# Performance work log

Measured on AMD Instinct MI355X. Metric: run time of the kernel, lower is better.

The kernel has to match this reference:

```python
import jax, jax.numpy as jnp
import numpy as np
from jax.scipy.special import logsumexp


def _lstm(x, mask, Wk, Wr, b, reverse=False):
    # x: [B,T,D], mask: [B,T] bool. Keras LSTM defaults: gate order i,f,g,o,
    # sigmoid recurrent activation, tanh activation. Masked steps carry state.
    if reverse:
        x = x[:, ::-1]
        mask = mask[:, ::-1]
    B, T, _ = x.shape
    H = Wr.shape[0]
    xz = jnp.einsum('btd,dh->bth', x, Wk) + b  # [B,T,4H] input projections, done once

    def step(carry, inp):
        h, c = carry
        z_t, m = inp  # [B,4H], [B]
        z = z_t + h @ Wr
        i, f, g, o = jnp.split(z, 4, axis=-1)
        i = jax.nn.sigmoid(i)
        f = jax.nn.sigmoid(f)
        g = jnp.tanh(g)
        o = jax.nn.sigmoid(o)
        c_new = f * c + i * g
        h_new = o * jnp.tanh(c_new)
        m = m[:, None]
        h = jnp.where(m, h_new, h)
        c = jnp.where(m, c_new, c)
        return (h, c), h

    h0 = jnp.zeros((B, H), x.dtype)
    (_, _), hs = jax.lax.scan(step, (h0, h0), (xz.transpose(1, 0, 2), mask.T))
    hs = hs.transpose(1, 0, 2)  # [B,T,H]
    if reverse:
        hs = hs[:, ::-1]
    return hs


def _crf_log_likelihood(logits, tags, lengths, trans):
    # TFA crf_log_likelihood: sequence_score - log_norm (forward algorithm)
    B, T, C = logits.shape
    t_idx = jnp.arange(T)
    mask = t_idx[None, :] < lengths[:, None]  # [B,T]
    # unary score: sum_t logits[b,t,tags[b,t]] over valid t
    unary = jnp.take_along_axis(logits, tags[..., None], axis=2)[..., 0]
    unary = jnp.sum(jnp.where(mask, unary, 0.0), axis=1)
    # binary score: sum_t trans[tags[t], tags[t+1]] for t < len-1
    binary = trans[tags[:, :-1], tags[:, 1:]]  # [B,T-1]
    mask2 = t_idx[None, : T - 1] < (lengths - 1)[:, None]
    binary = jnp.sum(jnp.where(mask2, binary, 0.0), axis=1)
    # log normalizer via forward algorithm scan
    alpha0 = logits[:, 0]  # [B,C]

    def step(alpha, inp):
        logit_t, m = inp  # [B,C], [B]
        new = logsumexp(alpha[:, :, None] + trans[None], axis=1) + logit_t
        alpha = jnp.where(m[:, None], new, alpha)
        return alpha, None

    alpha, _ = jax.lax.scan(step, alpha0,
                            (logits[:, 1:].transpose(1, 0, 2), mask[:, 1:].T))
    log_norm = logsumexp(alpha, axis=1)
    return unary + binary - log_norm


def setup_inputs() -> dict:
    key = jax.random.key(0)
    ks = jax.random.split(key, 12)
    V, D, H, C, B, T = 30000, 300, 256, 9, 64, 512
    lengths = jax.random.randint(ks[0], (B,), T // 4, T + 1).astype(jnp.int32)
    valid = jnp.arange(T)[None, :] < lengths[:, None]
    inputs = (jax.random.randint(ks[1], (B, T), 1, V) * valid).astype(jnp.int32)
    targets = (jax.random.randint(ks[2], (B, T), 0, C) * valid).astype(jnp.int32)
    s = 0.05
    return {
        'inputs': inputs,
        'inputs_length': lengths,
        'targets': targets,
        'embedding': jax.random.normal(ks[3], (V, D), jnp.float32) * s,
        'Wk_f': jax.random.normal(ks[4], (D, 4 * H), jnp.float32) * s,
        'Wr_f': jax.random.normal(ks[5], (H, 4 * H), jnp.float32) * s,
        'b_f': jnp.zeros((4 * H,), jnp.float32),
        'Wk_b': jax.random.normal(ks[6], (D, 4 * H), jnp.float32) * s,
        'Wr_b': jax.random.normal(ks[7], (H, 4 * H), jnp.float32) * s,
        'b_b': jnp.zeros((4 * H,), jnp.float32),
        'dense_W': jax.random.normal(ks[8], (2 * H, C), jnp.float32) * s,
        'dense_b': jnp.zeros((C,), jnp.float32),
        'trans': jax.random.uniform(ks[9], (C, C), jnp.float32),
    }


def reference(inputs, inputs_length, targets, embedding, Wk_f, Wr_f, b_f,
              Wk_b, Wr_b, b_b, dense_W, dense_b, trans):
    T = inputs.shape[1]
    mask = jnp.arange(T)[None, :] < inputs_length[:, None]  # [B,T]
    emb = embedding[inputs]  # [B,T,D] (dropout is identity in inference)
    h_f = _lstm(emb, mask, Wk_f, Wr_f, b_f, reverse=False)
    h_b = _lstm(emb, mask, Wk_b, Wr_b, b_b, reverse=True)
    h = jnp.concatenate([h_f, h_b], axis=-1)  # [B,T,2H]
    logits = h @ dense_W + dense_b  # [B,T,C]
    log_likelihood = _crf_log_likelihood(logits, targets, inputs_length, trans)
    return logits, log_likelihood, trans
```

## Files before the change

### kernel.cpp

```cpp
#include <hip/hip_runtime.h>
#include <cstdint>
#include <cstddef>

typedef unsigned int  u32;
typedef unsigned short u16;
typedef _Float16 f16;
typedef _Float16 f16x2 __attribute__((ext_vector_type(2)));
typedef _Float16 half8 __attribute__((ext_vector_type(8)));
typedef float    f32x4v __attribute__((ext_vector_type(4)));
typedef int      i32x4 __attribute__((ext_vector_type(4)));

#define BATCH 64
#define TSEQ  512
#define DEMB  300
#define KPAD  320
#define HDIM  256
#define G4    1024
#define NCLS  9

__device__ __forceinline__ u32 packf16(float a, float b) {
  f16x2 v; v.x = (f16)a; v.y = (f16)b;
  return __builtin_bit_cast(u32, v);
}
__device__ __forceinline__ float f16f(u16 x) {
  return (float)__builtin_bit_cast(f16, x);
}
__device__ __forceinline__ float sigm_fast(float x) {
  return __builtin_amdgcn_rcpf(1.f + __expf(-x));
}
__device__ __forceinline__ float tanh_fast(float x) {
  float ax = __builtin_fabsf(x);
  float e = __expf(-2.f * ax);
  float t = (1.f - e) * __builtin_amdgcn_rcpf(1.f + e);
  return copysignf(t, x);
}

__global__ __launch_bounds__(256) void prep_k(
    const float* __restrict__ emb, u16* __restrict__ embf16,
    const float* __restrict__ Wk_f, const float* __restrict__ Wk_b,
    u16* __restrict__ wkt,
    const float* __restrict__ Wr_f, const float* __restrict__ Wr_b,
    signed char* __restrict__ wr8)
{
  const int bid = blockIdx.x;
  if (bid < 1875) {
    const int v  = bid * 16 + (threadIdx.x >> 4);
    const int kc = threadIdx.x & 15;
    uint2* __restrict__ dst = (uint2*)(embf16 + (size_t)v * KPAD + kc * 20);
    if (kc < 15) {
      const float4* __restrict__ src =
          (const float4*)(emb + (size_t)v * DEMB + kc * 20);
      float4 t0 = src[0], t1 = src[1], t2 = src[2], t3 = src[3], t4 = src[4];
      dst[0] = make_uint2(packf16(t0.x, t0.y), packf16(t0.z, t0.w));
      dst[1] = make_uint2(packf16(t1.x, t1.y), packf16(t1.z, t1.w));
      dst[2] = make_uint2(packf16(t2.x, t2.y), packf16(t2.z, t2.w));
      dst[3] = make_uint2(packf16(t3.x, t3.y), packf16(t3.z, t3.w));
      dst[4] = make_uint2(packf16(t4.x, t4.y), packf16(t4.z, t4.w));
    } else {
#pragma unroll
      for (int j = 0; j < 5; ++j) dst[j] = make_uint2(0u, 0u);
    }
    return;
  }
  const int t   = bid - 1875;
  const int dir = t >> 6;
  const int blk = t & 63;
  {
    const float* __restrict__ Wk = dir ? Wk_b : Wk_f;
    const int col = blk * 16 + (threadIdx.x >> 4);
    const int kc  = threadIdx.x & 15;
    u32* __restrict__ dst = (u32*)(wkt + ((size_t)dir * G4 + col) * KPAD + kc * 20);
    if (kc < 15) {
      float tmp[20];
#pragma unroll
      for (int j = 0; j < 20; ++j) tmp[j] = Wk[(size_t)(kc * 20 + j) * G4 + col];
#pragma unroll
      for (int j = 0; j < 10; ++j) dst[j] = packf16(tmp[2 * j], tmp[2 * j + 1]);
    } else {
#pragma unroll
      for (int j = 0; j < 10; ++j) dst[j] = 0u;
    }
  }
  {
    const float* __restrict__ Wr = dir ? Wr_b : Wr_f;
    const int col = blk * 16 + (threadIdx.x >> 4);
    const int k0  = (threadIdx.x & 15) * 16;
    float tmp[16];
#pragma unroll
    for (int j = 0; j < 16; ++j) tmp[j] = Wr[(size_t)(k0 + j) * G4 + col];
    u32 pw[4];
#pragma unroll
    for (int jj = 0; jj < 4; ++jj) {
      u32 p = 0;
#pragma unroll
      for (int b = 0; b < 4; ++b) {
        int q = (int)__builtin_rintf(tmp[4 * jj + b] * 512.f);
        q = q > 127 ? 127 : (q < -127 ? -127 : q);
        p |= ((u32)(q & 255)) << (8 * b);
      }
      pw[jj] = p;
    }
    *(uint4*)(wr8 + ((size_t)dir * G4 + col) * HDIM + k0) =
        make_uint4(pw[0], pw[1], pw[2], pw[3]);
  }
}

__global__ __launch_bounds__(256, 2) void xz_gemm_k(
    const int* __restrict__ inputs, const u16* __restrict__ wkt,
    const u16* __restrict__ embf16, const float* __restrict__ b_f,
    const float* __restrict__ b_b, u16* __restrict__ xz)
{
  __shared__ __align__(16) u16 Bs[64 * 328];
  const int tid  = threadIdx.x;
  const int wv   = tid >> 6, lane = tid & 63;
  const int quad = lane >> 4, fl = lane & 15;
  const int rb   = blockIdx.x * 64;

  {
    const int srow = tid >> 2, seg = (tid & 3) * 80;
    const int vrow = inputs[rb + srow];
    const u16* __restrict__ bsrc = embf16 + (size_t)vrow * KPAD + seg;
#pragma unroll
    for (int jj = 0; jj < 10; ++jj) {
      uint4 v = *(const uint4*)(bsrc + jj * 8);
      *(uint4*)&Bs[srow * 328 + seg + jj * 8] = v;
    }
  }
  __syncthreads();

#pragma unroll
  for (int grp = 0; grp < 4; ++grp) {
    f32x4v acc[4][2][4];
#pragma unroll
    for (int d = 0; d < 4; ++d)
#pragma unroll
      for (int i = 0; i < 2; ++i)
#pragma unroll
        for (int bt = 0; bt < 4; ++bt) acc[d][i][bt] = (f32x4v){0.f, 0.f, 0.f, 0.f};

#pragma unroll
    for (int kt = 0; kt < 10; ++kt) {
      half8 bf[4];
#pragma unroll
      for (int bt = 0; bt < 4; ++bt)
        bf[bt] = *(const half8*)&Bs[(bt * 16 + fl) * 328 + kt * 32 + quad * 8];
#pragma unroll
      for (int d = 0; d < 4; ++d) {
        const int dcb = grp * 4 + d;
        const int dir = dcb >> 3;
        const int cb1 = (dcb & 7) * 128;
        const u16* __restrict__ arow =
            wkt + ((size_t)(dir * G4) + cb1 + wv * 32 + fl) * KPAD + quad * 8;
#pragma unroll
        for (int i = 0; i < 2; ++i) {
          half8 af = *(const half8*)(arow + (size_t)(i * 16) * KPAD + kt * 32);
#pragma unroll
          for (int bt = 0; bt < 4; ++bt)
            acc[d][i][bt] = __builtin_amdgcn_mfma_f32_16x16x32_f16(
                af, bf[bt], acc[d][i][bt], 0, 0, 0);
        }
      }
    }

#pragma unroll
    for (int d = 0; d < 4; ++d) {
      const int dcb = grp * 4 + d;
      const int dir = dcb >> 3;
      const int cb1 = (dcb & 7) * 128;
      const float* __restrict__ bias = dir ? b_b : b_f;
#pragma unroll
      for (int bt = 0; bt < 4; ++bt) {
        const int row = rb + bt * 16 + fl;
        u16* __restrict__ orow = xz + ((size_t)(dir * BATCH * TSEQ) + row) * G4;
#pragma unroll
        for (int i = 0; i < 2; ++i) {
          const int mb = cb1 + wv * 32 + i * 16 + quad * 4;
          const float4 bb = *(const float4*)&bias[mb];
          f32x4v v = acc[d][i][bt];
          uint2 pk;
          pk.x = packf16(v[0] + bb.x, v[1] + bb.y);
          pk.y = packf16(v[2] + bb.z, v[3] + bb.w);
          *(uint2*)&orow[mb] = pk;
        }
      }
    }
  }
}

#define MFI(a, b, c) __builtin_amdgcn_mfma_i32_16x16x64_i8(a, b, c, 0, 0, 0)
#define LD8(g, ct, kc) (*(const i32x4*)(wr8w + (size_t)((g) * 256 + 32 * w + (ct) * 16 + l15) * HDIM + (kc) * 64 + q16))
#define DECL8(g, ct) \
  i32x4 W##g##ct##_0 = LD8(g, ct, 0), W##g##ct##_1 = LD8(g, ct, 1), \
        W##g##ct##_2 = LD8(g, ct, 2), W##g##ct##_3 = LD8(g, ct, 3); \
  asm volatile("" : "+a"(W##g##ct##_0), "+a"(W##g##ct##_1), \
                    "+a"(W##g##ct##_2), "+a"(W##g##ct##_3));
#define TILE(g, ct) \
  i32x4 ac##g##ct = (i32x4){0, 0, 0, 0}; \
  ac##g##ct = MFI(af0, W##g##ct##_0, ac##g##ct); \
  ac##g##ct = MFI(af1, W##g##ct##_1, ac##g##ct); \
  ac##g##ct = MFI(af2, W##g##ct##_2, ac##g##ct); \
  ac##g##ct = MFI(af3, W##g##ct##_3, ac##g##ct);

__global__ __launch_bounds__(512, 2) void lstm_k(
    const u16* __restrict__ xz, const signed char* __restrict__ wr8,
    const int* __restrict__ lengths, u16* __restrict__ hcat)
{
  const int chain = blockIdx.x;
  const int dir   = chain >> 6;
  const int batch = chain & 63;
  const int tid  = threadIdx.x;
  const int w    = tid >> 6;
  const int lane = tid & 63;
  const int quad = lane >> 4, l15 = lane & 15;
  const int q16  = quad * 16;
  const int ctsel = quad & 1;
  const int j    = 32 * w + ctsel * 16 + l15;
  const int wr   = quad < 2;
  const float DEQ = 1.f / (512.f * 127.f);

  __shared__ __align__(16) signed char hpk[2][256];

  const signed char* __restrict__ wr8w = wr8 + (size_t)dir * G4 * HDIM;

  DECL8(0, 0) DECL8(0, 1) DECL8(1, 0) DECL8(1, 1)
  DECL8(2, 0) DECL8(2, 1) DECL8(3, 0) DECL8(3, 1)

  if (tid < 256) hpk[0][tid] = 0;

  float c = 0.f, h = 0.f;
  const int len = lengths[batch];
  const u16* __restrict__ xzb = xz + (size_t)(dir * BATCH + batch) * TSEQ * G4;
  u16* __restrict__ hrow = hcat + (size_t)batch * TSEQ * 512 + dir * 256;
  __syncthreads();

  int tt = dir ? (TSEQ - 1) : 0;
  const int dt = dir ? -1 : 1;
  u16 x0 = xzb[(size_t)tt * G4 + j];
  u16 x1 = xzb[(size_t)tt * G4 + 256 + j];
  u16 x2 = xzb[(size_t)tt * G4 + 512 + j];
  u16 x3 = xzb[(size_t)tt * G4 + 768 + j];

  for (int st = 0; st < TSEQ; ++st) {
    const int ttn = (st == TSEQ - 1) ? tt : tt + dt;
    u16 xn0 = xzb[(size_t)ttn * G4 + j];
    u16 xn1 = xzb[(size_t)ttn * G4 + 256 + j];
    u16 xn2 = xzb[(size_t)ttn * G4 + 512 + j];
    u16 xn3 = xzb[(size_t)ttn * G4 + 768 + j];

    const int par = st & 1;
    const signed char* hb = &hpk[par][0];
    i32x4 af0 = *(const i32x4*)(hb + q16);
    i32x4 af1 = *(const i32x4*)(hb + 64 + q16);
    i32x4 af2 = *(const i32x4*)(hb + 128 + q16);
    i32x4 af3 = *(const i32x4*)(hb + 192 + q16);

    TILE(0, 0) TILE(0, 1)
    TILE(1, 0) TILE(1, 1)
    TILE(2, 0) TILE(2, 1)
    TILE(3, 0) TILE(3, 1)

    int ri = ctsel ? ac01[0] : ac00[0];
    int rf = ctsel ? ac11[0] : ac10[0];
    int rg = ctsel ? ac21[0] : ac20[0];
    int ro = ctsel ? ac31[0] : ac30[0];

    float zi = (float)ri * DEQ + f16f(x0);
    float zf = (float)rf * DEQ + f16f(x1);
    float zg = (float)rg * DEQ + f16f(x2);
    float zo = (float)ro * DEQ + f16f(x3);
    float ig = sigm_fast(zi);
    float fg = sigm_fast(zf);
    float gg = tanh_fast(zg);
    float og = sigm_fast(zo);
    float cn = fg * c + ig * gg;
    float hn = og * tanh_fast(cn);
    if (tt < len) { c = cn; h = hn; }
    if (wr) {
      u32 hb2 = packf16(h, h);
      hrow[(size_t)tt * 512 + j] = (u16)(hb2 & 0xffffu);
      int hq = (int)__builtin_rintf(h * 127.f);
      hpk[par ^ 1][j] = (signed char)hq;
    }
    __syncthreads();
    x0 = xn0; x1 = xn1; x2 = xn2; x3 = xn3; tt = ttn;
  }
}

__global__ __launch_bounds__(256) void dense_k(
    const u16* __restrict__ hcat, const float* __restrict__ W,
    const float* __restrict__ bias, float* __restrict__ out)
{
  const int lane = threadIdx.x & 63;
  const int wv = threadIdx.x >> 6;
  const int rowbase = (blockIdx.x * 4 + wv) * 8;
  for (int rr = 0; rr < 8; ++rr) {
    const int row = rowbase + rr;
    const u16* __restrict__ hr = hcat + (size_t)row * 512;
    float hv[8];
#pragma unroll
    for (int i = 0; i < 8; ++i)
      hv[i] = f16f(hr[i * 64 + lane]);
    float myout = 0.f;
#pragma unroll
    for (int cc = 0; cc < 9; ++cc) {
      float p = 0.f;
#pragma unroll
      for (int i = 0; i < 8; ++i)
        p = fmaf(hv[i], W[(size_t)(i * 64 + lane) * 9 + cc], p);
#pragma unroll
      for (int o = 32; o > 0; o >>= 1) p += __shfl_xor(p, o);
      if (lane == cc) myout = p + bias[cc];
    }
    if (lane < 9) out[(size_t)row * 9 + lane] = myout;
  }
}

__global__ __launch_bounds__(64) void crf_k(
    const float* __restrict__ logits, const int* __restrict__ tags,
    const int* __restrict__ lengths, const float* __restrict__ trans,
    float* __restrict__ out_ll, float* __restrict__ out_trans)
{
  const int b = blockIdx.x;
  const int lane = threadIdx.x;
  const int len = lengths[b];
  const float* __restrict__ lg = logits + (size_t)b * TSEQ * NCLS;
  const int* __restrict__ tg = tags + (size_t)b * TSEQ;

  float ua = 0.f, ba = 0.f;
  for (int t = lane; t < TSEQ; t += 64) {
    int tag = tg[t];
    if (t < len) ua += lg[t * 9 + tag];
    if (t < len - 1) ba += trans[tag * 9 + tg[t + 1]];
  }
  float s = ua + ba;
#pragma unroll
  for (int o = 32; o > 0; o >>= 1) s += __shfl_xor(s, o);

  const int j = (lane < 9) ? lane : 0;
  float trc[9], alpha[9];
#pragma unroll
  for (int i = 0; i < 9; ++i) trc[i] = trans[i * 9 + j];
#pragma unroll
  for (int i = 0; i < 9; ++i) alpha[i] = lg[i];
  for (int t = 1; t < TSEQ; ++t) {
    if (t >= len) break;
    float m = -1e30f;
#pragma unroll
    for (int i = 0; i < 9; ++i) m = fmaxf(m, alpha[i] + trc[i]);
    float ss = 0.f;
#pragma unroll
    for (int i = 0; i < 9; ++i) ss += __expf(alpha[i] + trc[i] - m);
    float nj = __logf(ss) + m + lg[t * 9 + j];
#pragma unroll
    for (int i = 0; i < 9; ++i) alpha[i] = __shfl(nj, i);
  }
  float m2 = -1e30f;
#pragma unroll
  for (int i = 0; i < 9; ++i) m2 = fmaxf(m2, alpha[i]);
  float s2 = 0.f;
#pragma unroll
  for (int i = 0; i < 9; ++i) s2 += __expf(alpha[i] - m2);
  float lse = __logf(s2) + m2;
  if (lane == 0) out_ll[b] = s - lse;
  if (b == 0)
    for (int i = lane; i < 81; i += 64) out_trans[i] = trans[i];
}

extern "C" void kernel_launch(void* const* d_in, const int* in_sizes, int n_in,
                              void* d_out, int out_size, void* d_ws, size_t ws_size,
                              hipStream_t stream)
{
  const int*   inputs  = (const int*)d_in[0];
  const int*   lengths = (const int*)d_in[1];
  const int*   targets = (const int*)d_in[2];
  const float* emb     = (const float*)d_in[3];
  const float* Wk_f    = (const float*)d_in[4];
  const float* Wr_f    = (const float*)d_in[5];
  const float* b_f     = (const float*)d_in[6];
  const float* Wk_b    = (const float*)d_in[7];
  const float* Wr_b    = (const float*)d_in[8];
  const float* b_b     = (const float*)d_in[9];
  const float* dense_W = (const float*)d_in[10];
  const float* dense_b = (const float*)d_in[11];
  const float* trans   = (const float*)d_in[12];

  char* ws = (char*)d_ws;
  u16*         wkt    = (u16*)ws;
  signed char* wr8    = (signed char*)(ws + 1310720ull);
  u16*         embf16 = (u16*)(ws + 1835008ull);
  u16*         xz     = (u16*)(ws + 1835008ull + 19200000ull);
  u16*         hcat   = (u16*)(ws + 1835008ull + 19200000ull + 134217728ull);

  float* out_logits = (float*)d_out;
  float* out_ll     = out_logits + (size_t)BATCH * TSEQ * NCLS;
  float* out_trans  = out_ll + BATCH;

  hipLaunchKernelGGL(prep_k, dim3(2003), dim3(256), 0, stream,
                     emb, embf16, Wk_f, Wk_b, wkt, Wr_f, Wr_b, wr8);
  hipLaunchKernelGGL(xz_gemm_k, dim3(512), dim3(256), 0, stream,
                     inputs, wkt, embf16, b_f, b_b, xz);
  hipLaunchKernelGGL(lstm_k, dim3(128), dim3(512), 0, stream,
                     xz, wr8, lengths, hcat);
  hipLaunchKernelGGL(dense_k, dim3(1024), dim3(256), 0, stream,
                     hcat, dense_W, dense_b, out_logits);
  hipLaunchKernelGGL(crf_k, dim3(64), dim3(64), 0, stream,
                     out_logits, targets, lengths, trans, out_ll, out_trans);
}
```

Baseline: 745.0 us.

## Restructure xz GEMM with LDS double-buffered weights, lighter LSTM barrier, LDS dense weights

The input-projection GEMM now runs 128-row blocks of 512 threads. Weight tiles are staged through a double-buffered LDS array with a register prefetch of the next tile, instead of each wave reading weights straight from global memory. The LSTM step loop replaces __syncthreads with a raw s_waitcnt lgkmcnt(0) plus s_barrier, which skips the wait on outstanding global memory operations. The dense kernel copies the 512x9 weight matrix into LDS once per block. The risks are a barrier on every k-step in the GEMM, fewer blocks, and the weaker barrier, which relies on the global stores not being needed before the next step.

Measured after the change: 740.2 us. Within noise of the previous version (-0.6%).

```diff
diff --git a/kernel.cpp b/kernel.cpp
--- a/kernel.cpp
+++ b/kernel.cpp
@@ -17,6 +17,8 @@
 #define HDIM  256
 #define G4    1024
 #define NCLS  9
+
+#define BARRIER_LDS() asm volatile("s_waitcnt lgkmcnt(0)\n\ts_barrier" ::: "memory")
 
 __device__ __forceinline__ u32 packf16(float a, float b) {
   f16x2 v; v.x = (f16)a; v.y = (f16)b;
@@ -105,84 +107,82 @@
   }
 }
 
-__global__ __launch_bounds__(256, 2) void xz_gemm_k(
+__global__ __launch_bounds__(512) void xz_gemm_k(
     const int* __restrict__ inputs, const u16* __restrict__ wkt,
     const u16* __restrict__ embf16, const float* __restrict__ b_f,
     const float* __restrict__ b_b, u16* __restrict__ xz)
 {
-  __shared__ __align__(16) u16 Bs[64 * 328];
+  __shared__ __align__(16) u16 Bs[128 * 328];
+  __shared__ __align__(16) u16 As[2][128 * 40];
   const int tid  = threadIdx.x;
   const int wv   = tid >> 6, lane = tid & 63;
   const int quad = lane >> 4, fl = lane & 15;
-  const int rb   = blockIdx.x * 64;
+  const int rb   = blockIdx.x * 128;
 
   {
-    const int srow = tid >> 2, seg = (tid & 3) * 80;
-    const int vrow = inputs[rb + srow];
+    const int row = tid >> 2, seg = (tid & 3) * 80;
+    const int vrow = inputs[rb + row];
     const u16* __restrict__ bsrc = embf16 + (size_t)vrow * KPAD + seg;
-#pragma unroll
-    for (int jj = 0; jj < 10; ++jj) {
-      uint4 v = *(const uint4*)(bsrc + jj * 8);
-      *(uint4*)&Bs[srow * 328 + seg + jj * 8] = v;
-    }
+    u16* __restrict__ bdst = &Bs[row * 328 + seg];
+#pragma unroll
+    for (int j = 0; j < 10; ++j)
+      *(uint4*)(bdst + j * 8) = *(const uint4*)(bsrc + j * 8);
+  }
+  const int acol = tid >> 2, aseg = (tid & 3) * 8;
+  {
+    const u16* __restrict__ asrc = wkt + (size_t)acol * KPAD + aseg;
+    *(uint4*)&As[0][acol * 40 + aseg] = *(const uint4*)(asrc);
   }
   __syncthreads();
 
-#pragma unroll
-  for (int grp = 0; grp < 4; ++grp) {
-    f32x4v acc[4][2][4];
-#pragma unroll
-    for (int d = 0; d < 4; ++d)
-#pragma unroll
-      for (int i = 0; i < 2; ++i)
-#pragma unroll
-        for (int bt = 0; bt < 4; ++bt) acc[d][i][bt] = (f32x4v){0.f, 0.f, 0.f, 0.f};
+  for (int cb = 0; cb < 16; ++cb) {
+    const int dir = cb >> 3;
+    const int cb1 = (cb & 7) * 128;
+    const float* __restrict__ bias = dir ? b_b : b_f;
+    f32x4v acc[8];
+#pragma unroll
+    for (int bt = 0; bt < 8; ++bt) acc[bt] = (f32x4v){0.f, 0.f, 0.f, 0.f};
 
 #pragma unroll
     for (int kt = 0; kt < 10; ++kt) {
-      half8 bf[4];
-#pragma unroll
-      for (int bt = 0; bt < 4; ++bt)
+      const int it  = cb * 10 + kt;
+      const int cur = it & 1;
+      const int ncb = (kt == 9) ? cb + 1 : cb;
+      const int nkt = (kt == 9) ? 0 : kt + 1;
+      const bool have_next = (kt < 9) || (cb < 15);
+      uint4 nav;
+      if (have_next) {
+        const int ndir = ncb >> 3;
+        const int ncb1 = (ncb & 7) * 128;
+        nav = *(const uint4*)(wkt + ((size_t)(ndir * G4) + ncb1 + acol) * KPAD
+                              + nkt * 32 + aseg);
+      }
+
+      half8 af = *(const half8*)&As[cur][(wv * 16 + fl) * 40 + quad * 8];
+      half8 bf[8];
+#pragma unroll
+      for (int bt = 0; bt < 8; ++bt)
         bf[bt] = *(const half8*)&Bs[(bt * 16 + fl) * 328 + kt * 32 + quad * 8];
 #pragma unroll
-      for (int d = 0; d < 4; ++d) {
-        const int dcb = grp * 4 + d;
-        const int dir = dcb >> 3;
-        const int cb1 = (dcb & 7) * 128;
-        const u16* __restrict__ arow =
-            wkt + ((size_t)(dir * G4) + cb1 + wv * 32 + fl) * KPAD + quad * 8;
-#pragma unroll
-        for (int i = 0; i < 2; ++i) {
-          half8 af = *(const half8*)(arow + (size_t)(i * 16) * KPAD + kt * 32);
-#pragma unroll
-          for (int bt = 0; bt < 4; ++bt)
-            acc[d][i][bt] = __builtin_amdgcn_mfma_f32_16x16x32_f16(
-                af, bf[bt], acc[d][i][bt], 0, 0, 0);
-        }
-      }
-    }
-
-#pragma unroll
-    for (int d = 0; d < 4; ++d) {
-      const int dcb = grp * 4 + d;
-      const int dir = dcb >> 3;
-      const int cb1 = (dcb & 7) * 128;
-      const float* __restrict__ bias = dir ? b_b : b_f;
-#pragma unroll
-      for (int bt = 0; bt < 4; ++bt) {
-        const int row = rb + bt * 16 + fl;
-        u16* __restrict__ orow = xz + ((size_t)(dir * BATCH * TSEQ) + row) * G4;
-#pragma unroll
-        for (int i = 0; i < 2; ++i) {
-          const int mb = cb1 + wv * 32 + i * 16 + quad * 4;
-          const float4 bb = *(const float4*)&bias[mb];
-          f32x4v v = acc[d][i][bt];
-          uint2 pk;
-          pk.x = packf16(v[0] + bb.x, v[1] + bb.y);
-          pk.y = packf16(v[2] + bb.z, v[3] + bb.w);
-          *(uint2*)&orow[mb] = pk;
-        }
-      }
+      for (int bt = 0; bt < 8; ++bt)
+        acc[bt] = __builtin_amdgcn_mfma_f32_16x16x32_f16(af, bf[bt], acc[bt], 0, 0, 0);
+
+      if (have_next)
+        *(uint4*)&As[cur ^ 1][acol * 40 + aseg] = nav;
+      BARRIER_LDS();
+    }
+
+#pragma unroll
+    for (int bt = 0; bt < 8; ++bt) {
+      const int row = rb + bt * 16 + fl;
+      u16* __restrict__ orow = xz + ((size_t)(dir * BATCH * TSEQ) + row) * G4;
+      const int mb = cb1 + wv * 16 + quad * 4;
+      const float4 bb = *(const float4*)&bias[mb];
+      f32x4v v = acc[bt];
+      uint2 pk;
+      pk.x = packf16(v[0] + bb.x, v[1] + bb.y);
+      pk.y = packf16(v[2] + bb.z, v[3] + bb.w);
+      *(uint2*)&orow[mb] = pk;
     }
   }
 }
@@ -281,7 +281,7 @@
       int hq = (int)__builtin_rintf(h * 127.f);
       hpk[par ^ 1][j] = (signed char)hq;
     }
-    __syncthreads();
+    BARRIER_LDS();
     x0 = xn0; x1 = xn1; x2 = xn2; x3 = xn3; tt = ttn;
   }
 }
@@ -290,6 +290,10 @@
     const u16* __restrict__ hcat, const float* __restrict__ W,
     const float* __restrict__ bias, float* __restrict__ out)
 {
+  __shared__ float Wlds[512 * 9];
+  for (int s = threadIdx.x; s < 512 * 9; s += 256) Wlds[s] = W[s];
+  __syncthreads();
+
   const int lane = threadIdx.x & 63;
   const int wv = threadIdx.x >> 6;
   const int rowbase = (blockIdx.x * 4 + wv) * 8;
@@ -306,7 +310,7 @@
       float p = 0.f;
 #pragma unroll
       for (int i = 0; i < 8; ++i)
-        p = fmaf(hv[i], W[(size_t)(i * 64 + lane) * 9 + cc], p);
+        p = fmaf(hv[i], Wlds[(i * 64 + lane) * 9 + cc], p);
 #pragma unroll
       for (int o = 32; o > 0; o >>= 1) p += __shfl_xor(p, o);
       if (lane == cc) myout = p + bias[cc];
@@ -397,7 +401,7 @@
 
   hipLaunchKernelGGL(prep_k, dim3(2003), dim3(256), 0, stream,
                      emb, embf16, Wk_f, Wk_b, wkt, Wr_f, Wr_b, wr8);
-  hipLaunchKernelGGL(xz_gemm_k, dim3(512), dim3(256), 0, stream,
+  hipLaunchKernelGGL(xz_gemm_k, dim3(256), dim3(512), 0, stream,
                      inputs, wkt, embf16, b_f, b_b, xz);
   hipLaunchKernelGGL(lstm_k, dim3(128), dim3(512), 0, stream,
                      xz, wr8, lengths, hcat);
```
